# Performance work log

Hardware: AMD Instinct MI355X
Metric: run time of the kernel (lower is better)

Reference implementation:

```python
import jax, jax.numpy as jnp
import numpy as np

B, C, T, F = 8, 256, 256, 128
D, H, HEADS, K = 64, 128, 4, 8
I = D * K  # unfold channel dim = D*8


def _conv2d(x, w, b, stride=1, pad=0):
    y = jax.lax.conv_general_dilated(x, w, (stride, stride), [(pad, pad), (pad, pad)],
                                     dimension_numbers=('NCHW', 'OIHW', 'NCHW'))
    return y + b[None, :, None, None]


def _convT(x, w, b, strides):
    y = jax.lax.conv_transpose(x, w, strides, 'VALID', dimension_numbers=('NCHW', 'OIHW', 'NCHW'))
    return y + b[None, :, None, None]


def _sru_dir(x, Wx, bf, br, Whw):
    # x: (N, L, I). SRU: all matmuls precomputed, only elementwise recurrence in scan.
    u = jnp.einsum('nli,ih->nlh', x, Wx)  # (N, L, 3H)
    xt, fp, rp = jnp.split(u, 3, axis=-1)
    f = jax.nn.sigmoid(fp + bf)
    r = jax.nn.sigmoid(rp + br)
    xhw = jnp.einsum('nli,ih->nlh', x, Whw)  # highway projection (I != H)

    def step(c, inp):
        xt_t, f_t, r_t, xhw_t = inp
        c = f_t * c + (1.0 - f_t) * xt_t
        h = r_t * c + (1.0 - r_t) * xhw_t
        return c, h

    c0 = jnp.zeros((x.shape[0], bf.shape[-1]), x.dtype)
    seq = tuple(jnp.swapaxes(a, 0, 1) for a in (xt, f, r, xhw))  # (L, N, H)
    _, hs = jax.lax.scan(step, c0, seq)
    return jnp.swapaxes(hs, 0, 1)  # (N, L, H)


def _sru_bidir(x, Wx, bf, br, Whw):
    hf = _sru_dir(x, Wx[0], bf[0], br[0], Whw[0])
    hb = _sru_dir(x[:, ::-1], Wx[1], bf[1], br[1], Whw[1])[:, ::-1]
    return jnp.concatenate([hf, hb], axis=-1)  # (N, L, 2H)


def _unfold_last(x, k):
    # nn.Unfold(kernel=(1,k)) over last axis: (B,D,T,F) -> (B, D*k, T, F-k+1)
    L = x.shape[-1] - k + 1
    p = jnp.stack([x[..., i:i + L] for i in range(k)], axis=2)  # (B, D, k, T, L)
    b, d = x.shape[0], x.shape[1]
    return p.reshape(b, d * k, x.shape[2], L)


def _pathway(ag, Wx, bf, br, Whw, pw, pb, ctw, ctb):
    # unfold -> bidirectional SRU over last axis -> proj -> ConvTranspose2d(I->D, kernel (1,8))
    b, d, t, f = ag.shape
    L = f - K + 1
    u = _unfold_last(ag, K)                                  # (B, I, t, L)
    seq = u.transpose(0, 2, 3, 1).reshape(b * t, L, d * K)   # scan along unfolded axis
    h = _sru_bidir(seq, Wx, bf, br, Whw)                     # (b*t, L, 2H)
    z = h @ pw + pb                                          # (b*t, L, I)
    z = z.reshape(b, t, L, d * K).transpose(0, 3, 1, 2)      # (B, I, t, L)
    return _convT(z, ctw, ctb, (1, 1))                       # (B, D, t, f)


def _attention(x, qkv_w, qkv_b, ow, ob):
    b, d, t, f = x.shape
    n = t * f
    tok = x.reshape(b, d, n).transpose(0, 2, 1)  # (B, N, D)
    qkv = tok @ qkv_w + qkv_b
    q, k, v = jnp.split(qkv, 3, axis=-1)
    dh = d // HEADS
    sp = lambda a: a.reshape(b, n, HEADS, dh).transpose(0, 2, 1, 3)
    q, k, v = sp(q), sp(k), sp(v)
    s = jnp.einsum('bhnd,bhmd->bhnm', q, k) / jnp.sqrt(jnp.asarray(dh, x.dtype))
    a = jax.nn.softmax(s, axis=-1)
    o = jnp.einsum('bhnm,bhmd->bhnd', a, v).transpose(0, 2, 1, 3).reshape(b, n, d)
    o = o @ ow + ob
    return o.transpose(0, 2, 1).reshape(b, d, t, f)


def _forward(A, compress_w, compress_b, down_w0, down_b0, down_w1, down_b1,
             f_Wx, f_bf, f_br, f_Whw, f_proj_w, f_proj_b, f_ct_w, f_ct_b,
             t_Wx, t_bf, t_br, t_Whw, t_proj_w, t_proj_b, t_ct_w, t_ct_b,
             qkv_w, qkv_b, out_w, out_b, up_w0, up_b0, up_w1, up_b1, final_w, final_b):
    # Compressor: 1x1 conv C->D then 2 strided downsample units
    x0 = _conv2d(A, compress_w, compress_b)                              # (B,D,T,F)
    x1 = jax.nn.relu(_conv2d(x0, down_w0, down_b0, stride=2, pad=1))     # (B,D,T/2,F/2)
    x2 = jax.nn.relu(_conv2d(x1, down_w1, down_b1, stride=2, pad=1))     # (B,D,T/4,F/4)
    ag = x2
    # Dual path: frequency scan then time scan, with residuals as in _dual_path
    freq_out = _pathway(ag, f_Wx, f_bf, f_br, f_Whw, f_proj_w, f_proj_b, f_ct_w, f_ct_b) + ag
    agt = ag.transpose(0, 1, 3, 2)  # scan over time axis
    time_out = _pathway(agt, t_Wx, t_bf, t_br, t_Whw, t_proj_w, t_proj_b, t_ct_w, t_ct_b).transpose(0, 1, 3, 2) + freq_out
    # TF self-attention with residual
    dp = _attention(time_out, qkv_w, qkv_b, out_w, out_b) + time_out
    # U-Net style reconstruction with skips, project back to C
    y = _convT(dp, up_w0, up_b0, (2, 2)) + x1
    y = _convT(y, up_w1, up_b1, (2, 2)) + x0
    return _conv2d(y, final_w, final_b)                                  # (B,C,T,F)


def setup_inputs() -> dict:
    key = jax.random.key(0)
    ks = iter(jax.random.split(key, 64))

    def p(shape, scale=0.05):
        return jax.random.normal(next(ks), shape, dtype=jnp.float32) * scale

    inp = dict(
        A=jax.random.normal(next(ks), (B, C, T, F), dtype=jnp.float32),
        compress_w=p((D, C, 1, 1)), compress_b=p((D,)),
        down_w0=p((D, D, 3, 3)), down_b0=p((D,)),
        down_w1=p((D, D, 3, 3)), down_b1=p((D,)),
        f_Wx=p((2, I, 3 * H)), f_bf=p((2, H)), f_br=p((2, H)), f_Whw=p((2, I, H)),
        f_proj_w=p((2 * H, I)), f_proj_b=p((I,)), f_ct_w=p((D, I, 1, K)), f_ct_b=p((D,)),
        t_Wx=p((2, I, 3 * H)), t_bf=p((2, H)), t_br=p((2, H)), t_Whw=p((2, I, H)),
        t_proj_w=p((2 * H, I)), t_proj_b=p((I,)), t_ct_w=p((D, I, 1, K)), t_ct_b=p((D,)),
        qkv_w=p((D, 3 * D)), qkv_b=p((3 * D,)), out_w=p((D, D)), out_b=p((D,)),
        up_w0=p((D, D, 2, 2)), up_b0=p((D,)),
        up_w1=p((D, D, 2, 2)), up_b1=p((D,)),
        final_w=p((C, D, 1, 1)), final_b=p((C,)),
    )
    return inp


def reference(A, compress_w, compress_b, down_w0, down_b0, down_w1, down_b1,
              f_Wx, f_bf, f_br, f_Whw, f_proj_w, f_proj_b, f_ct_w, f_ct_b,
              t_Wx, t_bf, t_br, t_Whw, t_proj_w, t_proj_b, t_ct_w, t_ct_b,
              qkv_w, qkv_b, out_w, out_b, up_w0, up_b0, up_w1, up_b1, final_w, final_b):
    return _forward(A, compress_w, compress_b, down_w0, down_b0, down_w1, down_b1,
                    f_Wx, f_bf, f_br, f_Whw, f_proj_w, f_proj_b, f_ct_w, f_ct_b,
                    t_Wx, t_bf, t_br, t_Whw, t_proj_w, t_proj_b, t_ct_w, t_ct_b,
                    qkv_w, qkv_b, out_w, out_b, up_w0, up_b0, up_w1, up_b1, final_w, final_b)
```

## Files before the change

kernel.cpp:

```cpp
#include <hip/hip_runtime.h>

#define BB 8
#define CC 256
#define TT 256
#define FF 128
#define DD 64
#define HH 128
#define NHEADS 4
#define KK 8
#define II 512
#define T2 128
#define F2 64
#define T4 64
#define F4 32
#define P4 2048

#define LF 25
#define LT 57
#define MF (512*LF)
#define MT (256*LT)

typedef __attribute__((ext_vector_type(8))) short bf16x8;
typedef __attribute__((ext_vector_type(4))) float f32x4;

__device__ __forceinline__ ushort f2b(float x) {
    unsigned u = __float_as_uint(x);
    unsigned r = (u + 0x7FFFu + ((u >> 16) & 1u)) >> 16;
    return (ushort)r;
}
__device__ __forceinline__ float b2f(ushort x) {
    return __uint_as_float(((unsigned)x) << 16);
}
__device__ __forceinline__ unsigned cvtpk_bf16(float lo, float hi) {
    unsigned r;
    asm("v_cvt_pk_bf16_f32 %0, %1, %2" : "=v"(r) : "v"(lo), "v"(hi));
    return r;
}

__global__ __launch_bounds__(256) void pack_all_k(
    const float* __restrict__ cw, const float* __restrict__ fw,
    const float* __restrict__ upw0, const float* __restrict__ upw1,
    const float* __restrict__ qkv_w, const float* __restrict__ ow,
    const float* __restrict__ dw0, const float* __restrict__ dw1,
    const float* __restrict__ f_pw, const float* __restrict__ t_pw,
    const float* __restrict__ f_ctw, const float* __restrict__ t_ctw,
    const float* __restrict__ f_Wx, const float* __restrict__ f_Whw,
    const float* __restrict__ t_Wx, const float* __restrict__ t_Whw,
    ushort* __restrict__ cw16, ushort* __restrict__ fw16,
    ushort* __restrict__ WupT0, ushort* __restrict__ WupT1,
    ushort* __restrict__ qkvwT, ushort* __restrict__ owT,
    ushort* __restrict__ WT9d0, ushort* __restrict__ WT9d1,
    ushort* __restrict__ pwF16, ushort* __restrict__ pwT16,
    ushort* __restrict__ WctF, ushort* __restrict__ WctT_,
    ushort* __restrict__ WcatF, ushort* __restrict__ WcatTm)
{
    int bid = blockIdx.x, tid = threadIdx.x;
    if (bid < 64)        { int g = bid * 256 + tid; cw16[g] = f2b(cw[g]); return; }
    if (bid < 128)       { int g = (bid - 64) * 256 + tid; fw16[g] = f2b(fw[g]); return; }
    if (bid < 256) {
        const float* w = (bid < 192) ? upw0 : upw1;
        ushort* O = (bid < 192) ? WupT0 : WupT1;
        int g = ((bid - 128) & 63) * 256 + tid;
        int c = g & 63; int n = g >> 6;
        int parity = n >> 6, d = n & 63;
        O[g] = f2b(w[((d * 64 + c) * 2 + (1 - (parity >> 1))) * 2 + (1 - (parity & 1))]);
        return;
    }
    if (bid < 304) {
        int g = (bid - 256) * 256 + tid;
        int k = g & 63, n = g >> 6;
        qkvwT[g] = f2b(qkv_w[k * 192 + n]); return;
    }
    if (bid < 320) {
        int g = (bid - 304) * 256 + tid;
        int k = g & 63, n = g >> 6;
        owT[g] = f2b(ow[k * 64 + n]); return;
    }
    if (bid < 608) {
        const float* w = (bid < 464) ? dw0 : dw1;
        ushort* O = (bid < 464) ? WT9d0 : WT9d1;
        int g = ((bid - 320) % 144) * 256 + tid;
        int c = g & 63; int rest = g >> 6;
        int d = rest & 63; int tap = rest >> 6;
        O[g] = f2b(w[(d * 64 + c) * 9 + tap]); return;
    }
    if (bid < 1632) {
        const float* w = (bid < 1120) ? f_pw : t_pw;
        ushort* O = (bid < 1120) ? pwF16 : pwT16;
        int g = ((bid - 608) % 512) * 256 + tid;
        O[g] = f2b(w[g]); return;
    }
    if (bid < 3680) {
        const float* ctw = (bid < 2656) ? f_ctw : t_ctw;
        ushort* O = (bid < 2656) ? WctF : WctT_;
        int g = ((bid - 1632) % 1024) * 256 + tid;
        int k = g & 511; int n = g >> 9;
        int tap = n >> 6, d = n & 63;
        O[g] = f2b(ctw[((d * 512) + k) * 8 + tap]); return;
    }
    {
        const float* Wx  = (bid < 5728) ? f_Wx  : t_Wx;
        const float* Whw = (bid < 5728) ? f_Whw : t_Whw;
        ushort* O = (bid < 5728) ? WcatF : WcatTm;
        int g = ((bid - 3680) % 2048) * 256 + tid;
        int k = g & 511; int n = g >> 9;
        int dir = n >> 9; int c = n & 511;
        float v = (c < 384) ? Wx[(dir * 512 + k) * 384 + c]
                            : Whw[(dir * 512 + k) * 128 + (c - 384)];
        O[g] = f2b(v);
    }
}

__global__ __launch_bounds__(256) void w3_gemm_k(
    const ushort* __restrict__ pwA, const ushort* __restrict__ wctA,
    const ushort* __restrict__ pwB, const ushort* __restrict__ wctB,
    ushort* __restrict__ w3A, ushort* __restrict__ w3B)
{
    const int M = 256, K = 512;
    const ushort* A16  = blockIdx.z ? pwB  : pwA;
    const ushort* BT16 = blockIdx.z ? wctB : wctA;
    ushort* C16        = blockIdx.z ? w3B  : w3A;
    __shared__ ushort As[128][40];
    __shared__ ushort Bs[128][40];
    int m0 = blockIdx.y * 128, n0 = blockIdx.x * 128;
    int tid = threadIdx.x;
    int wave = tid >> 6, lane = tid & 63;
    int wm = (wave & 1) * 64, wn = (wave >> 1) * 64;
    int l15 = lane & 15, lhi = lane >> 4;
    f32x4 acc[4][4] = {};
    int rs = tid >> 2, qs = tid & 3;

    for (int k0 = 0; k0 < K; k0 += 32) {
        *(uint4*)&As[rs][qs * 8]      = *(const uint4*)(A16 + (long long)(m0 + rs) * K + k0 + qs * 8);
        *(uint4*)&As[rs + 64][qs * 8] = *(const uint4*)(A16 + (long long)(m0 + rs + 64) * K + k0 + qs * 8);
        *(uint4*)&Bs[rs][qs * 8]      = *(const uint4*)(BT16 + (long long)(n0 + rs) * K + k0 + qs * 8);
        *(uint4*)&Bs[rs + 64][qs * 8] = *(const uint4*)(BT16 + (long long)(n0 + rs + 64) * K + k0 + qs * 8);
        __syncthreads();
        bf16x8 af[4], bfr[4];
#pragma unroll
        for (int fr = 0; fr < 4; ++fr)
            af[fr] = *(const bf16x8*)&As[wm + fr * 16 + l15][lhi * 8];
#pragma unroll
        for (int fc = 0; fc < 4; ++fc)
            bfr[fc] = *(const bf16x8*)&Bs[wn + fc * 16 + l15][lhi * 8];
#pragma unroll
        for (int fr = 0; fr < 4; ++fr)
#pragma unroll
            for (int fc = 0; fc < 4; ++fc)
                acc[fr][fc] = __builtin_amdgcn_mfma_f32_16x16x32_bf16(af[fr], bfr[fc], acc[fr][fc], 0, 0, 0);
        __syncthreads();
    }
#pragma unroll
    for (int fr = 0; fr < 4; ++fr)
#pragma unroll
        for (int fc = 0; fc < 4; ++fc) {
            int col = n0 + wn + fc * 16 + l15;
#pragma unroll
            for (int r = 0; r < 4; ++r) {
                int row = m0 + wm + fr * 16 + lhi * 4 + r;
                C16[(long long)col * M + row] = f2b(acc[fr][fc][r]);
            }
        }
}

__global__ void bias3_red_k(const float* __restrict__ pbF, const float* __restrict__ ctwF,
                            const float* __restrict__ pbT, const float* __restrict__ ctwT,
                            float* __restrict__ b3F, float* __restrict__ b3T)
{
    int n = blockIdx.x; int path = blockIdx.y;
    const float* pb  = path ? pbT  : pbF;
    const float* ctw = path ? ctwT : ctwF;
    float* b3        = path ? b3T  : b3F;
    int d = n & 63, tap = n >> 6;
    int tid = threadIdx.x;
    float s = 0.f;
    for (int i = tid; i < 512; i += 256)
        s += pb[i] * ctw[(d * 512 + i) * 8 + tap];
    __shared__ float red[256];
    red[tid] = s; __syncthreads();
    for (int st = 128; st > 0; st >>= 1) {
        if (tid < st) red[tid] += red[tid + st];
        __syncthreads();
    }
    if (tid == 0) b3[n] = red[0];
}

__global__ void unfold_both_k(const float* __restrict__ ag,
                              ushort* __restrict__ uF, ushort* __restrict__ uT)
{
    long long gid = (long long)blockIdx.x * blockDim.x + threadIdx.x;
    if (gid < (long long)MF * II) {
        int ch = (int)(gid & 511); int row = (int)(gid >> 9);
        int b = row / (T4 * LF); int rem = row - b * (T4 * LF);
        int t = rem / LF; int l = rem - t * LF;
        int d = ch >> 3, i = ch & 7;
        uF[gid] = f2b(ag[((long long)((b * DD + d) * T4 + t)) * F4 + l + i]);
    } else {
        long long g2 = gid - (long long)MF * II;
        int ch = (int)(g2 & 511); int row = (int)(g2 >> 9);
        int b = row / (F4 * LT); int rem = row - b * (F4 * LT);
        int tt = rem / LT; int l = rem - tt * LT;
        int d = ch >> 3, i = ch & 7;
        uT[g2] = f2b(ag[((long long)((b * DD + d) * T4 + (l + i))) * F4 + tt]);
    }
}

__global__ __launch_bounds__(256) void gates_fused_k(
    const ushort* __restrict__ uF, const ushort* __restrict__ uT,
    const ushort* __restrict__ WF, const ushort* __restrict__ WTm,
    float* __restrict__ GxtF, float* __restrict__ GxhF,
    ushort* __restrict__ GfF, ushort* __restrict__ GrF,
    float* __restrict__ GxtT, float* __restrict__ GxhT,
    ushort* __restrict__ GfT, ushort* __restrict__ GrT,
    const float* __restrict__ f_bf, const float* __restrict__ f_br,
    const float* __restrict__ t_bf, const float* __restrict__ t_br)
{
    __shared__ ushort As[128][40];
    __shared__ ushort Bs[128][40];
    const int K = 512;
    int by = blockIdx.y;
    bool tp = by >= 100;
    const ushort* A16 = tp ? uT : uF;
    const ushort* WT  = tp ? WTm : WF;
    float* Gxt = tp ? GxtT : GxtF;
    float* Gxh = tp ? GxhT : GxhF;
    ushort* Gf = tp ? GfT : GfF;
    ushort* Gr = tp ? GrT : GrF;
    const float* bfw = tp ? t_bf : f_bf;
    const float* brw = tp ? t_br : f_br;
    int m0 = (tp ? by - 100 : by) * 128;
    int n0 = blockIdx.x * 128;
    int tid = threadIdx.x, wave = tid >> 6, lane = tid & 63;
    int wm = (wave & 1) * 64, wn = (wave >> 1) * 64;
    int l15 = lane & 15, lhi = lane >> 4;
    f32x4 acc[4][4] = {};
    int rs = tid >> 2, qs = tid & 3;

    for (int k0 = 0; k0 < K; k0 += 32) {
        *(uint4*)&As[rs][qs * 8]      = *(const uint4*)(A16 + (long long)(m0 + rs) * K + k0 + qs * 8);
        *(uint4*)&As[rs + 64][qs * 8] = *(const uint4*)(A16 + (long long)(m0 + rs + 64) * K + k0 + qs * 8);
        *(uint4*)&Bs[rs][qs * 8]      = *(const uint4*)(WT + (long long)(n0 + rs) * K + k0 + qs * 8);
        *(uint4*)&Bs[rs + 64][qs * 8] = *(const uint4*)(WT + (long long)(n0 + rs + 64) * K + k0 + qs * 8);
        __syncthreads();
        bf16x8 af[4], bfr[4];
#pragma unroll
        for (int fr = 0; fr < 4; ++fr)
            af[fr] = *(const bf16x8*)&As[wm + fr * 16 + l15][lhi * 8];
#pragma unroll
        for (int fc = 0; fc < 4; ++fc)
            bfr[fc] = *(const bf16x8*)&Bs[wn + fc * 16 + l15][lhi * 8];
#pragma unroll
        for (int fr = 0; fr < 4; ++fr)
#pragma unroll
            for (int fc = 0; fc < 4; ++fc)
                acc[fr][fc] = __builtin_amdgcn_mfma_f32_16x16x32_bf16(af[fr], bfr[fc], acc[fr][fc], 0, 0, 0);
        __syncthreads();
    }
#pragma unroll
    for (int fc = 0; fc < 4; ++fc) {
        int col = n0 + wn + fc * 16 + l15;
        int dir = col >> 9, c = col & 511;
        int cls = c >> 7, h = c & 127;
        int dh = dir * 128 + h;
#pragma unroll
        for (int fr = 0; fr < 4; ++fr) {
#pragma unroll
            for (int r = 0; r < 4; ++r) {
                int row = m0 + wm + fr * 16 + lhi * 4 + r;
                long long idx = (long long)row * 256 + dh;
                float v = acc[fr][fc][r];
                if (cls == 0)      Gxt[idx] = v;
                else if (cls == 3) Gxh[idx] = v;
                else if (cls == 1) Gf[idx] = f2b(1.f / (1.f + __expf(-(v + bfw[dh]))));
                else               Gr[idx] = f2b(1.f / (1.f + __expf(-(v + brw[dh]))));
            }
        }
    }
}

__global__ void sru_scan_both_k(
    const float* __restrict__ GxtF, const float* __restrict__ GxhF,
    const ushort* __restrict__ GfF, const ushort* __restrict__ GrF,
    ushort* __restrict__ hF,
    const float* __restrict__ GxtT, const float* __restrict__ GxhT,
    const ushort* __restrict__ GfT, const ushort* __restrict__ GrT,
    ushort* __restrict__ hT)
{
    int gid = blockIdx.x * blockDim.x + threadIdx.x;
    const float *Gxt, *Gxh; const ushort *Gf, *Gr; ushort* hout; int L;
    if (gid < 512 * 256) {
        Gxt = GxtF; Gxh = GxhF; Gf = GfF; Gr = GrF; hout = hF; L = LF;
    } else {
        gid -= 512 * 256;
        Gxt = GxtT; Gxh = GxhT; Gf = GfT; Gr = GrT; hout = hT; L = LT;
    }
    int h = gid & 127; int dir = (gid >> 7) & 1; int n = gid >> 8;
    int dh = dir * 128 + h;
    float c = 0.f;
    for (int s = 0; s < L; ++s) {
        int l = dir ? (L - 1 - s) : s;
        long long off = (long long)(n * L + l) * 256 + dh;
        float xt = Gxt[off], xh = Gxh[off];
        float f = b2f(Gf[off]);
        float r = b2f(Gr[off]);
        c = f * c + (1.f - f) * xt;
        float hv = r * c + (1.f - r) * xh;
        hout[off] = f2b(hv);
    }
}

__global__ __launch_bounds__(256) void gemmW_both_k(
    const ushort* __restrict__ hF, const ushort* __restrict__ W3F,
    float* __restrict__ YF, const float* __restrict__ b3F,
    const ushort* __restrict__ hT, const ushort* __restrict__ W3T,
    float* __restrict__ YT, const float* __restrict__ b3T)
{
    __shared__ ushort As[128][40];
    __shared__ ushort Bs[128][40];
    const int N = 512, K = 256;
    int by = blockIdx.y;
    bool tp = by >= 100;
    const ushort* A16 = tp ? hT : hF;
    const ushort* WT  = tp ? W3T : W3F;
    float* C          = tp ? YT : YF;
    const float* bias = tp ? b3T : b3F;
    int m0 = (tp ? by - 100 : by) * 128;
    int n0 = blockIdx.x * 128;
    int tid = threadIdx.x, wave = tid >> 6, lane = tid & 63;
    int wm = (wave & 1) * 64, wn = (wave >> 1) * 64;
    int l15 = lane & 15, lhi = lane >> 4;
    f32x4 acc[4][4] = {};
    int rs = tid >> 2, qs = tid & 3;

    for (int k0 = 0; k0 < K; k0 += 32) {
        *(uint4*)&As[rs][qs * 8]      = *(const uint4*)(A16 + (long long)(m0 + rs) * K + k0 + qs * 8);
        *(uint4*)&As[rs + 64][qs * 8] = *(const uint4*)(A16 + (long long)(m0 + rs + 64) * K + k0 + qs * 8);
        *(uint4*)&Bs[rs][qs * 8]      = *(const uint4*)(WT + (long long)(n0 + rs) * K + k0 + qs * 8);
        *(uint4*)&Bs[rs + 64][qs * 8] = *(const uint4*)(WT + (long long)(n0 + rs + 64) * K + k0 + qs * 8);
        __syncthreads();
        bf16x8 af[4], bfr[4];
#pragma unroll
        for (int fr = 0; fr < 4; ++fr)
            af[fr] = *(const bf16x8*)&As[wm + fr * 16 + l15][lhi * 8];
#pragma unroll
        for (int fc = 0; fc < 4; ++fc)
            bfr[fc] = *(const bf16x8*)&Bs[wn + fc * 16 + l15][lhi * 8];
#pragma unroll
        for (int fr = 0; fr < 4; ++fr)
#pragma unroll
            for (int fc = 0; fc < 4; ++fc)
                acc[fr][fc] = __builtin_amdgcn_mfma_f32_16x16x32_bf16(af[fr], bfr[fc], acc[fr][fc], 0, 0, 0);
        __syncthreads();
    }
#pragma unroll
    for (int fc = 0; fc < 4; ++fc) {
        int col = n0 + wn + fc * 16 + l15;
        float bv = bias[col];
#pragma unroll
        for (int fr = 0; fr < 4; ++fr) {
#pragma unroll
            for (int r = 0; r < 4; ++r) {
                int row = m0 + wm + fr * 16 + lhi * 4 + r;
                C[(long long)row * N + col] = acc[fr][fc][r] + bv;
            }
        }
    }
}

template<int BN>
__global__ __launch_bounds__(256) void mfma_nchw_k(
    const float* __restrict__ X, const ushort* __restrict__ WT,
    const float* __restrict__ bias, float* __restrict__ Y,
    int P, int N, int K)
{
    constexpr int FC = BN / 32;
    __shared__ ushort As[128][40];
    int p0 = blockIdx.x * 128;
    int n0 = blockIdx.y * BN;
    int b  = blockIdx.z;
    int tid = threadIdx.x, wave = tid >> 6, lane = tid & 63;
    int l15 = lane & 15, lhi = lane >> 4;
    int wm = (wave & 1) * 64, wn = (wave >> 1) * (BN / 2);
    f32x4 acc[4][FC] = {};
    const float* Xb = X + (long long)b * K * P;
    int kk_s = tid >> 3, pq_s = tid & 7;

    for (int k0 = 0; k0 < K; k0 += 32) {
        const float* xr = Xb + (long long)(k0 + kk_s) * P + p0;
#pragma unroll
        for (int j = 0; j < 4; ++j) {
            float4 v = *(const float4*)(xr + j * 32 + pq_s * 4);
            int pp = j * 32 + pq_s * 4;
            As[pp][kk_s]     = f2b(v.x);
            As[pp + 1][kk_s] = f2b(v.y);
            As[pp + 2][kk_s] = f2b(v.z);
            As[pp + 3][kk_s] = f2b(v.w);
        }
        __syncthreads();
        bf16x8 af[4], bfr[FC];
#pragma unroll
        for (int fr = 0; fr < 4; ++fr)
            af[fr] = *(const bf16x8*)&As[wm + fr * 16 + l15][lhi * 8];
#pragma unroll
        for (int fc = 0; fc < FC; ++fc)
            bfr[fc] = *(const bf16x8*)(WT + (long long)(n0 + wn + fc * 16 + l15) * K + k0 + lhi * 8);
#pragma unroll
        for (int fr = 0; fr < 4; ++fr)
#pragma unroll
            for (int fc = 0; fc < FC; ++fc)
                acc[fr][fc] = __builtin_amdgcn_mfma_f32_16x16x32_bf16(af[fr], bfr[fc], acc[fr][fc], 0, 0, 0);
        __syncthreads();
    }
#pragma unroll
    for (int fc = 0; fc < FC; ++fc) {
        int n = n0 + wn + fc * 16 + l15;
        float bv = bias[n];
        float* yr = Y + ((long long)(b * N + n)) * P + p0 + wm + lhi * 4;
#pragma unroll
        for (int fr = 0; fr < 4; ++fr) {
            float4 o;
            o.x = acc[fr][fc][0] + bv;
            o.y = acc[fr][fc][1] + bv;
            o.z = acc[fr][fc][2] + bv;
            o.w = acc[fr][fc][3] + bv;
            *(float4*)(yr + fr * 16) = o;
        }
    }
}

__global__ __launch_bounds__(256) void mfma_nchw16_k(
    const ushort* __restrict__ X, const ushort* __restrict__ WT,
    const float* __restrict__ bias, float* __restrict__ Y,
    int P, int N, int K)
{
    constexpr int BN = 128, FC = 4;
    __shared__ ushort As[128][40];
    int p0 = blockIdx.x * 128;
    int n0 = blockIdx.y * BN;
    int b  = blockIdx.z;
    int tid = threadIdx.x, wave = tid >> 6, lane = tid & 63;
    int l15 = lane & 15, lhi = lane >> 4;
    int wm = (wave & 1) * 64, wn = (wave >> 1) * (BN / 2);
    f32x4 acc[4][FC] = {};
    const ushort* Xb = X + (long long)b * K * P;
    int kk_s = tid >> 3, pq_s = tid & 7;

    for (int k0 = 0; k0 < K; k0 += 32) {
        const ushort* xr = Xb + (long long)(k0 + kk_s) * P + p0 + pq_s * 16;
#pragma unroll
        for (int j = 0; j < 2; ++j) {
            uint4 v = *(const uint4*)(xr + j * 8);
            const ushort* e = (const ushort*)&v;
            int pp = pq_s * 16 + j * 8;
#pragma unroll
            for (int t = 0; t < 8; ++t) As[pp + t][kk_s] = e[t];
        }
        __syncthreads();
        bf16x8 af[4], bfr[FC];
#pragma unroll
        for (int fr = 0; fr < 4; ++fr)
            af[fr] = *(const bf16x8*)&As[wm + fr * 16 + l15][lhi * 8];
#pragma unroll
        for (int fc = 0; fc < FC; ++fc)
            bfr[fc] = *(const bf16x8*)(WT + (long long)(n0 + wn + fc * 16 + l15) * K + k0 + lhi * 8);
#pragma unroll
        for (int fr = 0; fr < 4; ++fr)
#pragma unroll
            for (int fc = 0; fc < FC; ++fc)
                acc[fr][fc] = __builtin_amdgcn_mfma_f32_16x16x32_bf16(af[fr], bfr[fc], acc[fr][fc], 0, 0, 0);
        __syncthreads();
    }
#pragma unroll
    for (int fc = 0; fc < FC; ++fc) {
        int n = n0 + wn + fc * 16 + l15;
        float bv = bias[n];
        float* yr = Y + ((long long)(b * N + n)) * P + p0 + wm + lhi * 4;
#pragma unroll
        for (int fr = 0; fr < 4; ++fr) {
            float4 o;
            o.x = acc[fr][fc][0] + bv;
            o.y = acc[fr][fc][1] + bv;
            o.z = acc[fr][fc][2] + bv;
            o.w = acc[fr][fc][3] + bv;
            *(float4*)(yr + fr * 16) = o;
        }
    }
}

__global__ __launch_bounds__(256) void down_mfma_k(
    const float* __restrict__ in, const ushort* __restrict__ WT9,
    const float* __restrict__ bias, float* __restrict__ out,
    int Hi, int Wi)
{
    __shared__ ushort Is[289][64];
    int Ho = Hi >> 1, Wo = Wi >> 1;
    int ntx = Wo >> 3, nty = Ho >> 3;
    int tx = blockIdx.x % ntx; int rest = blockIdx.x / ntx;
    int ty = rest % nty; int b = rest / nty;
    int oy0 = ty * 8, ox0 = tx * 8;
    int iy0 = oy0 * 2 - 1, ix0 = ox0 * 2 - 1;
    int tid = threadIdx.x, wave = tid >> 6, lane = tid & 63;
    int l15 = lane & 15, lhi = lane >> 4;
    int wm = (wave & 1) * 32, wn = (wave >> 1) * 32;

    const float* ib = in + (long long)b * 64 * Hi * Wi;
    for (int i = tid; i < 289 * 64; i += 256) {
        int c = i / 289; int sp = i - c * 289;
        int r = sp / 17; int s = sp - r * 17;
        int iy = iy0 + r, ix = ix0 + s;
        float v = 0.f;
        if (iy >= 0 && iy < Hi && ix >= 0 && ix < Wi)
            v = ib[(long long)c * Hi * Wi + (long long)iy * Wi + ix];
        Is[sp][c ^ ((sp & 7) << 3)] = f2b(v);
    }
    __syncthreads();

    f32x4 acc[2][2] = {};
#pragma unroll
    for (int tap = 0; tap < 9; ++tap) {
        int kh = tap / 3, kw = tap - kh * 3;
#pragma unroll
        for (int half = 0; half < 2; ++half) {
            int c0 = half * 32 + lhi * 8;
            bf16x8 af[2], bw[2];
#pragma unroll
            for (int fr = 0; fr < 2; ++fr) {
                int p = wm + fr * 16 + l15;
                int sp = (2 * (p >> 3) + kh) * 17 + 2 * (p & 7) + kw;
                af[fr] = *(const bf16x8*)&Is[sp][c0 ^ ((sp & 7) << 3)];
            }
#pragma unroll
            for (int fc = 0; fc < 2; ++fc) {
                int d = wn + fc * 16 + l15;
                bw[fc] = *(const bf16x8*)(WT9 + (tap * 64 + d) * 64 + c0);
            }
#pragma unroll
            for (int fr = 0; fr < 2; ++fr)
#pragma unroll
                for (int fc = 0; fc < 2; ++fc)
                    acc[fr][fc] = __builtin_amdgcn_mfma_f32_16x16x32_bf16(af[fr], bw[fc], acc[fr][fc], 0, 0, 0);
        }
    }
#pragma unroll
    for (int fc = 0; fc < 2; ++fc) {
        int d = wn + fc * 16 + l15;
        float bv = bias[d];
        long long obase = ((long long)(b * 64 + d)) * Ho * Wo;
#pragma unroll
        for (int fr = 0; fr < 2; ++fr) {
#pragma unroll
            for (int r = 0; r < 4; ++r) {
                int p = wm + fr * 16 + lhi * 4 + r;
                int py = p >> 3, px = p & 7;
                out[obase + (long long)(oy0 + py) * Wo + ox0 + px] =
                    fmaxf(acc[fr][fc][r] + bv, 0.f);
            }
        }
    }
}

template<int OUT16>
__global__ __launch_bounds__(256) void up_mfma_k(
    const float* __restrict__ in, const ushort* __restrict__ WT,
    const float* __restrict__ bias, const float* __restrict__ resid,
    float* __restrict__ out, ushort* __restrict__ o16, int P, int wsh)
{
    __shared__ ushort As[128][72];
    int p0 = blockIdx.x * 128;
    int n0 = blockIdx.y * 128;
    int b  = blockIdx.z;
    int tid = threadIdx.x, wave = tid >> 6, lane = tid & 63;
    int l15 = lane & 15, lhi = lane >> 4;
    int wm = (wave & 1) * 64, wn = (wave >> 1) * 64;
    int Wi = 1 << wsh;
    int Ho = ((P >> wsh) << 1), Wo = Wi << 1;

    int kk_s = tid >> 3, pq_s = tid & 7;
#pragma unroll
    for (int h = 0; h < 2; ++h) {
        int k = h * 32 + kk_s;
        const float* xr = in + ((long long)(b * 64 + k)) * P + p0 + pq_s * 16;
#pragma unroll
        for (int j = 0; j < 4; ++j) {
            float4 v = *(const float4*)(xr + j * 4);
            int pp = pq_s * 16 + j * 4;
            As[pp][k]     = f2b(v.x);
            As[pp + 1][k] = f2b(v.y);
            As[pp + 2][k] = f2b(v.z);
            As[pp + 3][k] = f2b(v.w);
        }
    }
    __syncthreads();

    f32x4 acc[4][4] = {};
#pragma unroll
    for (int c = 0; c < 2; ++c) {
        bf16x8 af[4], bfr[4];
#pragma unroll
        for (int fr = 0; fr < 4; ++fr)
            af[fr] = *(const bf16x8*)&As[wm + fr * 16 + l15][c * 32 + lhi * 8];
#pragma unroll
        for (int fc = 0; fc < 4; ++fc)
            bfr[fc] = *(const bf16x8*)(WT + (long long)(n0 + wn + fc * 16 + l15) * 64 + c * 32 + lhi * 8);
#pragma unroll
        for (int fr = 0; fr < 4; ++fr)
#pragma unroll
            for (int fc = 0; fc < 4; ++fc)
                acc[fr][fc] = __builtin_amdgcn_mfma_f32_16x16x32_bf16(af[fr], bfr[fc], acc[fr][fc], 0, 0, 0);
    }

#pragma unroll
    for (int fc = 0; fc < 4; ++fc) {
        int n = n0 + wn + fc * 16 + l15;
        int parity = n >> 6, d = n & 63;
        int py = parity >> 1, px = parity & 1;
        float bv = bias[d];
        const long long obase = ((long long)(b * 64 + d)) * Ho * Wo;
#pragma unroll
        for (int fr = 0; fr < 4; ++fr) {
#pragma unroll
            for (int r = 0; r < 4; ++r) {
                int p = p0 + wm + fr * 16 + lhi * 4 + r;
                int iy = p >> wsh, ix = p & (Wi - 1);
                long long oi = obase + (long long)(2 * iy + py) * Wo + 2 * ix + px;
                float v = acc[fr][fc][r] + bv + resid[oi];
                if (OUT16) o16[oi] = f2b(v);
                else       out[oi] = v;
            }
        }
    }
}

__global__ __launch_bounds__(256) void mfma_qkv_k(
    const float* __restrict__ X, const ushort* __restrict__ WT,
    const float* __restrict__ bias, ushort* __restrict__ C16)
{
    __shared__ ushort As[128][72];
    int p0 = blockIdx.x * 128;
    int b  = blockIdx.z;
    int tid = threadIdx.x, wave = tid >> 6, lane = tid & 63;
    int l15 = lane & 15, lhi = lane >> 4;
    int wm = (wave & 1) * 64, wn = (wave >> 1) * 96;

    int kk_s = tid >> 3, pq_s = tid & 7;
#pragma unroll
    for (int h = 0; h < 2; ++h) {
        int k = h * 32 + kk_s;
        const float* xr = X + ((long long)(b * 64 + k)) * P4 + p0 + pq_s * 16;
#pragma unroll
        for (int j = 0; j < 4; ++j) {
            float4 v = *(const float4*)(xr + j * 4);
            int pp = pq_s * 16 + j * 4;
            As[pp][k]     = f2b(v.x);
            As[pp + 1][k] = f2b(v.y);
            As[pp + 2][k] = f2b(v.z);
            As[pp + 3][k] = f2b(v.w);
        }
    }
    __syncthreads();

    f32x4 acc[4][6] = {};
#pragma unroll
    for (int c = 0; c < 2; ++c) {
        bf16x8 af[4], bfr[6];
#pragma unroll
        for (int fr = 0; fr < 4; ++fr)
            af[fr] = *(const bf16x8*)&As[wm + fr * 16 + l15][c * 32 + lhi * 8];
#pragma unroll
        for (int fc = 0; fc < 6; ++fc)
            bfr[fc] = *(const bf16x8*)(WT + (long long)(wn + fc * 16 + l15) * 64 + c * 32 + lhi * 8);
#pragma unroll
        for (int fr = 0; fr < 4; ++fr)
#pragma unroll
            for (int fc = 0; fc < 6; ++fc)
                acc[fr][fc] = __builtin_amdgcn_mfma_f32_16x16x32_bf16(af[fr], bfr[fc], acc[fr][fc], 0, 0, 0);
    }
#pragma unroll
    for (int fc = 0; fc < 6; ++fc) {
        int n = wn + fc * 16 + l15;
        float bv = bias[n];
#pragma unroll
        for (int fr = 0; fr < 4; ++fr)
#pragma unroll
            for (int r = 0; r < 4; ++r) {
                int p = p0 + wm + fr * 16 + lhi * 4 + r;
                C16[((long long)(b * P4 + p)) * 192 + n] = f2b(acc[fr][fc][r] + bv);
            }
    }
}

__global__ __launch_bounds__(256) void mfma_attnout_k(
    const float* __restrict__ A, const ushort* __restrict__ owT,
    const float* __restrict__ ob, const float* __restrict__ resid,
    float* __restrict__ dp)
{
    __shared__ ushort As[128][72];
    int p0 = blockIdx.x * 128;
    int b  = blockIdx.z;
    int tid = threadIdx.x, wave = tid >> 6, lane = tid & 63;
    int l15 = lane & 15, lhi = lane >> 4;
    int wm = (wave & 1) * 64, wn = (wave >> 1) * 32;

    int rs = tid >> 2, qs = tid & 3;
#pragma unroll
    for (int h = 0; h < 2; ++h) {
        int row = h * 64 + rs;
        const float* ar = A + ((long long)(b * P4 + p0 + row)) * 64 + qs * 16;
#pragma unroll
        for (int j = 0; j < 4; ++j) {
            float4 v = *(const float4*)(ar + j * 4);
            int c = qs * 16 + j * 4;
            *(unsigned*)&As[row][c]     = cvtpk_bf16(v.x, v.y);
            *(unsigned*)&As[row][c + 2] = cvtpk_bf16(v.z, v.w);
        }
    }
    __syncthreads();

    f32x4 acc[4][2] = {};
#pragma unroll
    for (int c = 0; c < 2; ++c) {
        bf16x8 af[4], bfr[2];
#pragma unroll
        for (int fr = 0; fr < 4; ++fr)
            af[fr] = *(const bf16x8*)&As[wm + fr * 16 + l15][c * 32 + lhi * 8];
#pragma unroll
        for (int fc = 0; fc < 2; ++fc)
            bfr[fc] = *(const bf16x8*)(owT + (long long)(wn + fc * 16 + l15) * 64 + c * 32 + lhi * 8);
#pragma unroll
        for (int fr = 0; fr < 4; ++fr)
#pragma unroll
            for (int fc = 0; fc < 2; ++fc)
                acc[fr][fc] = __builtin_amdgcn_mfma_f32_16x16x32_bf16(af[fr], bfr[fc], acc[fr][fc], 0, 0, 0);
    }
#pragma unroll
    for (int fc = 0; fc < 2; ++fc) {
        int n = wn + fc * 16 + l15;
        float bv = ob[n];
        long long base = ((long long)(b * 64 + n)) * P4;
#pragma unroll
        for (int fr = 0; fr < 4; ++fr) {
            int p = p0 + wm + fr * 16 + lhi * 4;
            float4 rv = *(const float4*)(resid + base + p);
            float4 o;
            o.x = acc[fr][fc][0] + bv + rv.x;
            o.y = acc[fr][fc][1] + bv + rv.y;
            o.z = acc[fr][fc][2] + bv + rv.z;
            o.w = acc[fr][fc][3] + bv + rv.w;
            *(float4*)(dp + base + p) = o;
        }
    }
}

__global__ __launch_bounds__(256) void attn_mfma_k(const ushort* __restrict__ qkv,
                                                   float* __restrict__ out)
{
    __shared__ ushort Qs[128][40];
    __shared__ ushort Ks[64][40];
    __shared__ ushort VsT[16][72];
    __shared__ ushort Ps[128][72];
    int qt = blockIdx.x, h = blockIdx.y, b = blockIdx.z;
    int tid = threadIdx.x, wave = tid >> 6, lane = tid & 63;
    int l15 = lane & 15, lhi = lane >> 4;
    int q0 = wave * 32;

    for (int i = tid; i < 1024; i += 256) {
        int row = i >> 3, c = i & 7;
        *(unsigned*)&Qs[row][16 + c * 2] = 0u;
    }
    for (int i = tid; i < 512; i += 256) {
        int row = i >> 3, c = i & 7;
        *(unsigned*)&Ks[row][16 + c * 2] = 0u;
    }
    {
        const ushort* qp = qkv + ((long long)(b * P4 + qt * 128)) * 192 + h * 16;
        for (int i = tid; i < 2048; i += 256) {
            int row = i >> 4, d = i & 15;
            Qs[row][d] = f2b(b2f(qp[row * 192 + d]) * 0.25f);
        }
    }
    __syncthreads();

    float mmax[2] = {-1e30f, -1e30f};
    float lsum[2] = {0.f, 0.f};
    f32x4 oacc[2] = {};

    for (int k0 = 0; k0 < P4; k0 += 64) {
        const ushort* kp = qkv + ((long long)(b * P4 + k0)) * 192 + 64 + h * 16;
        for (int i = tid; i < 1024; i += 256) {
            int key = i >> 4, d = i & 15;
            Ks[key][d]  = kp[key * 192 + d];
            VsT[d][key] = kp[key * 192 + 64 + d];
        }
        __syncthreads();

        bf16x8 bq[2];
        bq[0] = *(const bf16x8*)&Qs[q0 + l15][lhi * 8];
        bq[1] = *(const bf16x8*)&Qs[q0 + 16 + l15][lhi * 8];
        f32x4 s[4][2];
#pragma unroll
        for (int fr = 0; fr < 4; ++fr) {
            bf16x8 ak = *(const bf16x8*)&Ks[fr * 16 + l15][lhi * 8];
            f32x4 z = {};
            s[fr][0] = __builtin_amdgcn_mfma_f32_16x16x32_bf16(ak, bq[0], z, 0, 0, 0);
            s[fr][1] = __builtin_amdgcn_mfma_f32_16x16x32_bf16(ak, bq[1], z, 0, 0, 0);
        }
#pragma unroll
        for (int fc = 0; fc < 2; ++fc) {
            float m = s[0][fc][0];
#pragma unroll
            for (int fr = 0; fr < 4; ++fr)
#pragma unroll
                for (int r = 0; r < 4; ++r) m = fmaxf(m, s[fr][fc][r]);
            m = fmaxf(m, __shfl_xor(m, 16));
            m = fmaxf(m, __shfl_xor(m, 32));
            float nm = fmaxf(mmax[fc], m);
            float corr = __expf(mmax[fc] - nm);
            mmax[fc] = nm;
            float ps = 0.f;
#pragma unroll
            for (int fr = 0; fr < 4; ++fr)
#pragma unroll
                for (int r = 0; r < 4; ++r) {
                    float p = __expf(s[fr][fc][r] - nm);
                    s[fr][fc][r] = p;
                    ps += p;
                }
            lsum[fc] = lsum[fc] * corr + ps;
#pragma unroll
            for (int r = 0; r < 4; ++r) oacc[fc][r] *= corr;
        }
#pragma unroll
        for (int fc = 0; fc < 2; ++fc)
#pragma unroll
            for (int fr = 0; fr < 4; ++fr) {
                uint2 pk;
                pk.x = cvtpk_bf16(s[fr][fc][0], s[fr][fc][1]);
                pk.y = cvtpk_bf16(s[fr][fc][2], s[fr][fc][3]);
                *(uint2*)&Ps[q0 + fc * 16 + l15][fr * 16 + lhi * 4] = pk;
            }
#pragma unroll
        for (int ks = 0; ks < 2; ++ks) {
            bf16x8 av = *(const bf16x8*)&VsT[l15][ks * 32 + lhi * 8];
#pragma unroll
            for (int fc = 0; fc < 2; ++fc) {
                bf16x8 bp = *(const bf16x8*)&Ps[q0 + fc * 16 + l15][ks * 32 + lhi * 8];
                oacc[fc] = __builtin_amdgcn_mfma_f32_16x16x32_bf16(av, bp, oacc[fc], 0, 0, 0);
            }
        }
        __syncthreads();
    }
#pragma unroll
    for (int fc = 0; fc < 2; ++fc) {
        float L = lsum[fc];
        L += __shfl_xor(L, 16);
        L += __shfl_xor(L, 32);
        float inv = 1.f / L;
        int q = qt * 128 + q0 + fc * 16 + l15;
        float* op = out + ((long long)(b * P4 + q)) * 64 + h * 16 + lhi * 4;
#pragma unroll
        for (int r = 0; r < 4; ++r) op[r] = oacc[fc][r] * inv;
    }
}

__global__ void convt_reduce_k(const float* __restrict__ Y, const float* __restrict__ bias,
                               const float* __restrict__ resid, float* __restrict__ out,
                               int NS, int L, int FO, int swap)
{
    int gid = blockIdx.x * blockDim.x + threadIdx.x;
    int total = BB * 64 * NS * FO;
    if (gid >= total) return;
    int d = gid & 63; int rest = gid >> 6;
    int p = rest % FO; rest /= FO;
    int s = rest % NS; int b = rest / NS;
    float v = bias[d];
    long long ybase = ((long long)(b * NS + s)) * L;
#pragma unroll
    for (int tap = 0; tap < 8; ++tap) {
        int l = p + tap - 7;
        if (l >= 0 && l < L) v += Y[(ybase + l) * 512 + tap * 64 + d];
    }
    long long oi = swap ? (((long long)(b * 64 + d) * FO + p) * NS + s)
                        : (((long long)(b * 64 + d) * NS + s) * FO + p);
    out[oi] = v + resid[oi];
}

extern "C" void kernel_launch(void* const* d_in, const int* in_sizes, int n_in,
                              void* d_out, int out_size, void* d_ws, size_t ws_size,
                              hipStream_t stream)
{
    const float* A_in  = (const float*)d_in[0];
    const float* cw    = (const float*)d_in[1];
    const float* cb    = (const float*)d_in[2];
    const float* dw0   = (const float*)d_in[3];
    const float* db0   = (const float*)d_in[4];
    const float* dw1   = (const float*)d_in[5];
    const float* db1   = (const float*)d_in[6];
    const float* f_Wx  = (const float*)d_in[7];
    const float* f_bf  = (const float*)d_in[8];
    const float* f_br  = (const float*)d_in[9];
    const float* f_Whw = (const float*)d_in[10];
    const float* f_pw  = (const float*)d_in[11];
    const float* f_pb  = (const float*)d_in[12];
    const float* f_ctw = (const float*)d_in[13];
    const float* f_ctb = (const float*)d_in[14];
    const float* t_Wx  = (const float*)d_in[15];
    const float* t_bf  = (const float*)d_in[16];
    const float* t_br  = (const float*)d_in[17];
    const float* t_Whw = (const float*)d_in[18];
    const float* t_pw  = (const float*)d_in[19];
    const float* t_pb  = (const float*)d_in[20];
    const float* t_ctw = (const float*)d_in[21];
    const float* t_ctb = (const float*)d_in[22];
    const float* qkv_w = (const float*)d_in[23];
    const float* qkv_b = (const float*)d_in[24];
    const float* ow    = (const float*)d_in[25];
    const float* ob    = (const float*)d_in[26];
    const float* upw0  = (const float*)d_in[27];
    const float* upb0  = (const float*)d_in[28];
    const float* upw1  = (const float*)d_in[29];
    const float* upb1  = (const float*)d_in[30];
    const float* fw    = (const float*)d_in[31];
    const float* fb    = (const float*)d_in[32];

    float* ws  = (float*)d_ws;
    float* out = (float*)d_out;

    float* ag    = ws + 0;
    float* x1    = ws + 1048576;
    float* uFf   = ws + 5242880;
    float* uTf   = ws + 8519680;
    float* GxtF  = ws + 12255232;
    float* GxhF  = ws + 15532032;
    float* GxtT  = ws + 18808832;
    float* GxhT  = ws + 22544384;
    float* GfFf  = ws + 26279936;
    float* GrFf  = ws + 27918336;
    float* GfTf  = ws + 29556736;
    float* GrTf  = ws + 31424512;
    float* hFf   = ws + 33292288;
    float* hTf   = ws + 34930688;
    float* YF    = ws + 5242880;
    float* YT    = ws + 11796480;
    float* y016f = ws + 19267584;
    float* y1    = ws + 5242880;
    float* pwFf  = ws + 36798464;
    float* pwTf  = ws + 36864000;
    float* w3Ff  = ws + 36929536;
    float* w3Tf  = ws + 36995072;
    float* b3Ff  = ws + 37060608;
    float* b3Tf  = ws + 37061120;
    float* wctFf = ws + 37061632;
    float* wctTf = ws + 37192704;
    float* wcaFf = ws + 37323776;
    float* wcaTf = ws + 37585920;
    float* cw16f = ws + 37848064;
    float* fw16f = ws + 37856256;
    float* wup0f = ws + 37864448;
    float* wup1f = ws + 37872640;
    float* qkvwf = ws + 37880832;
    float* owtf  = ws + 37886976;
    float* wdw0f = ws + 37889024;
    float* wdw1f = ws + 37907456;
    float* fout  = ws + 37925888;
    float* tout  = ws + 38974464;
    float* qkvbf = ws + 40023040;
    float* attnO = ws + 41595904;
    float* dp    = ws + 42644480;

    ushort* uF     = (ushort*)uFf;
    ushort* uT     = (ushort*)uTf;
    ushort* GfF    = (ushort*)GfFf;
    ushort* GrF    = (ushort*)GrFf;
    ushort* GfT    = (ushort*)GfTf;
    ushort* GrT    = (ushort*)GrTf;
    ushort* hF     = (ushort*)hFf;
    ushort* hT     = (ushort*)hTf;
    ushort* y016   = (ushort*)y016f;
    ushort* pwF16  = (ushort*)pwFf;
    ushort* pwT16  = (ushort*)pwTf;
    ushort* W3F    = (ushort*)w3Ff;
    ushort* W3T_   = (ushort*)w3Tf;
    ushort* WctF   = (ushort*)wctFf;
    ushort* WctT_  = (ushort*)wctTf;
    ushort* WcatF  = (ushort*)wcaFf;
    ushort* WcatTm = (ushort*)wcaTf;
    ushort* qkv16  = (ushort*)qkvbf;
    ushort* cw16   = (ushort*)cw16f;
    ushort* fw16   = (ushort*)fw16f;
    ushort* WupT0  = (ushort*)wup0f;
    ushort* WupT1  = (ushort*)wup1f;
    ushort* qkvwT  = (ushort*)qkvwf;
    ushort* owT    = (ushort*)owtf;
    ushort* WT9d0  = (ushort*)wdw0f;
    ushort* WT9d1  = (ushort*)wdw1f;
    float*  x0     = out;

    dim3 blk(256);

    pack_all_k<<<dim3(7776), blk, 0, stream>>>(
        cw, fw, upw0, upw1, qkv_w, ow, dw0, dw1, f_pw, t_pw, f_ctw, t_ctw,
        f_Wx, f_Whw, t_Wx, t_Whw,
        cw16, fw16, WupT0, WupT1, qkvwT, owT, WT9d0, WT9d1,
        pwF16, pwT16, WctF, WctT_, WcatF, WcatTm);
    w3_gemm_k<<<dim3(4, 2, 2), blk, 0, stream>>>(pwF16, WctF, pwT16, WctT_, W3F, W3T_);
    bias3_red_k<<<dim3(512, 2), blk, 0, stream>>>(f_pb, f_ctw, t_pb, t_ctw, b3Ff, b3Tf);

    mfma_nchw_k<64><<<dim3(256, 1, 8), blk, 0, stream>>>(A_in, cw16, cb, x0, 32768, 64, 256);

    down_mfma_k<<<dim3(1024), blk, 0, stream>>>(x0, WT9d0, db0, x1, TT, FF);
    down_mfma_k<<<dim3(256), blk, 0, stream>>>(x1, WT9d1, db1, ag, T2, F2);

    unfold_both_k<<<dim3(54784), blk, 0, stream>>>(ag, uF, uT);
    gates_fused_k<<<dim3(8, 214), blk, 0, stream>>>(uF, uT, WcatF, WcatTm,
        GxtF, GxhF, GfF, GrF, GxtT, GxhT, GfT, GrT, f_bf, f_br, t_bf, t_br);
    sru_scan_both_k<<<dim3(768), blk, 0, stream>>>(GxtF, GxhF, GfF, GrF, hF,
                                                   GxtT, GxhT, GfT, GrT, hT);
    gemmW_both_k<<<dim3(4, 214), blk, 0, stream>>>(hF, W3F, YF, b3Ff,
                                                   hT, W3T_, YT, b3Tf);
    convt_reduce_k<<<dim3(4096), blk, 0, stream>>>(YF, f_ctb, ag, fout, 64, LF, 32, 0);
    convt_reduce_k<<<dim3(4096), blk, 0, stream>>>(YT, t_ctb, fout, tout, 32, LT, 64, 1);

    mfma_qkv_k<<<dim3(16, 1, 8), blk, 0, stream>>>(tout, qkvwT, qkv_b, qkv16);
    attn_mfma_k<<<dim3(16, NHEADS, BB), blk, 0, stream>>>(qkv16, attnO);
    mfma_attnout_k<<<dim3(16, 1, 8), blk, 0, stream>>>(attnO, owT, ob, tout, dp);

    up_mfma_k<0><<<dim3(16, 2, 8), blk, 0, stream>>>(dp, WupT0, upb0, x1, y1, nullptr, 2048, 5);
    up_mfma_k<1><<<dim3(64, 2, 8), blk, 0, stream>>>(y1, WupT1, upb1, x0, nullptr, y016, 8192, 6);

    mfma_nchw16_k<<<dim3(256, 2, 8), blk, 0, stream>>>(y016, fw16, fb, out, 32768, 256, 64);
}
```

Baseline: 672.1 us.

## Store SRU gate and projection intermediates in bf16 and fuse both ConvT reductions

Changes the Gxt/Gxh gate outputs and the post-SRU projection outputs Y from fp32 to bf16, which halves their memory traffic in the gates, scan, gemm and reduce kernels. It also replaces the two sequential convt_reduce launches with one dual_reduce kernel that sums the frequency and time pathway contributions, both biases and the residual in a single pass. That removes the intermediate fout buffer and one launch. The cost is lower precision on values that were previously kept in fp32.

```diff
diff --git a/kernel.cpp b/kernel.cpp
--- a/kernel.cpp
+++ b/kernel.cpp
@@ -208,9 +208,9 @@
 __global__ __launch_bounds__(256) void gates_fused_k(
     const ushort* __restrict__ uF, const ushort* __restrict__ uT,
     const ushort* __restrict__ WF, const ushort* __restrict__ WTm,
-    float* __restrict__ GxtF, float* __restrict__ GxhF,
+    ushort* __restrict__ GxtF, ushort* __restrict__ GxhF,
     ushort* __restrict__ GfF, ushort* __restrict__ GrF,
-    float* __restrict__ GxtT, float* __restrict__ GxhT,
+    ushort* __restrict__ GxtT, ushort* __restrict__ GxhT,
     ushort* __restrict__ GfT, ushort* __restrict__ GrT,
     const float* __restrict__ f_bf, const float* __restrict__ f_br,
     const float* __restrict__ t_bf, const float* __restrict__ t_br)
@@ -222,8 +222,8 @@
     bool tp = by >= 100;
     const ushort* A16 = tp ? uT : uF;
     const ushort* WT  = tp ? WTm : WF;
-    float* Gxt = tp ? GxtT : GxtF;
-    float* Gxh = tp ? GxhT : GxhF;
+    ushort* Gxt = tp ? GxtT : GxtF;
+    ushort* Gxh = tp ? GxhT : GxhF;
     ushort* Gf = tp ? GfT : GfF;
     ushort* Gr = tp ? GrT : GrF;
     const float* bfw = tp ? t_bf : f_bf;
@@ -269,8 +269,8 @@
                 int row = m0 + wm + fr * 16 + lhi * 4 + r;
                 long long idx = (long long)row * 256 + dh;
                 float v = acc[fr][fc][r];
-                if (cls == 0)      Gxt[idx] = v;
-                else if (cls == 3) Gxh[idx] = v;
+                if (cls == 0)      Gxt[idx] = f2b(v);
+                else if (cls == 3) Gxh[idx] = f2b(v);
                 else if (cls == 1) Gf[idx] = f2b(1.f / (1.f + __expf(-(v + bfw[dh]))));
                 else               Gr[idx] = f2b(1.f / (1.f + __expf(-(v + brw[dh]))));
             }
@@ -279,15 +279,15 @@
 }
 
 __global__ void sru_scan_both_k(
-    const float* __restrict__ GxtF, const float* __restrict__ GxhF,
+    const ushort* __restrict__ GxtF, const ushort* __restrict__ GxhF,
     const ushort* __restrict__ GfF, const ushort* __restrict__ GrF,
     ushort* __restrict__ hF,
-    const float* __restrict__ GxtT, const float* __restrict__ GxhT,
+    const ushort* __restrict__ GxtT, const ushort* __restrict__ GxhT,
     const ushort* __restrict__ GfT, const ushort* __restrict__ GrT,
     ushort* __restrict__ hT)
 {
     int gid = blockIdx.x * blockDim.x + threadIdx.x;
-    const float *Gxt, *Gxh; const ushort *Gf, *Gr; ushort* hout; int L;
+    const ushort *Gxt, *Gxh, *Gf, *Gr; ushort* hout; int L;
     if (gid < 512 * 256) {
         Gxt = GxtF; Gxh = GxhF; Gf = GfF; Gr = GrF; hout = hF; L = LF;
     } else {
@@ -300,7 +300,7 @@
     for (int s = 0; s < L; ++s) {
         int l = dir ? (L - 1 - s) : s;
         long long off = (long long)(n * L + l) * 256 + dh;
-        float xt = Gxt[off], xh = Gxh[off];
+        float xt = b2f(Gxt[off]), xh = b2f(Gxh[off]);
         float f = b2f(Gf[off]);
         float r = b2f(Gr[off]);
         c = f * c + (1.f - f) * xt;
@@ -311,9 +311,9 @@
 
 __global__ __launch_bounds__(256) void gemmW_both_k(
     const ushort* __restrict__ hF, const ushort* __restrict__ W3F,
-    float* __restrict__ YF, const float* __restrict__ b3F,
+    ushort* __restrict__ YF, const float* __restrict__ b3F,
     const ushort* __restrict__ hT, const ushort* __restrict__ W3T,
-    float* __restrict__ YT, const float* __restrict__ b3T)
+    ushort* __restrict__ YT, const float* __restrict__ b3T)
 {
     __shared__ ushort As[128][40];
     __shared__ ushort Bs[128][40];
@@ -322,7 +322,7 @@
     bool tp = by >= 100;
     const ushort* A16 = tp ? hT : hF;
     const ushort* WT  = tp ? W3T : W3F;
-    float* C          = tp ? YT : YF;
+    ushort* C16       = tp ? YT : YF;
     const float* bias = tp ? b3T : b3F;
     int m0 = (tp ? by - 100 : by) * 128;
     int n0 = blockIdx.x * 128;
@@ -361,10 +361,32 @@
 #pragma unroll
             for (int r = 0; r < 4; ++r) {
                 int row = m0 + wm + fr * 16 + lhi * 4 + r;
-                C[(long long)row * N + col] = acc[fr][fc][r] + bv;
+                C16[(long long)row * N + col] = f2b(acc[fr][fc][r] + bv);
             }
         }
     }
+}
+
+__global__ void dual_reduce_k(const ushort* __restrict__ YF, const ushort* __restrict__ YT,
+                              const float* __restrict__ f_ctb, const float* __restrict__ t_ctb,
+                              const float* __restrict__ ag, float* __restrict__ tout)
+{
+    int gid = blockIdx.x * blockDim.x + threadIdx.x;
+    int d = gid & 63; int rest = gid >> 6;
+    int f = rest & 31; rest >>= 5;
+    int t = rest & 63; int b = rest >> 6;
+    float v = f_ctb[d] + t_ctb[d];
+    long long ybF = ((long long)(b * 64 + t)) * LF;
+    long long ybT = ((long long)(b * 32 + f)) * LT;
+#pragma unroll
+    for (int tap = 0; tap < 8; ++tap) {
+        int lf = f + tap - 7;
+        if (lf >= 0 && lf < LF) v += b2f(YF[(ybF + lf) * 512 + tap * 64 + d]);
+        int lt = t + tap - 7;
+        if (lt >= 0 && lt < LT) v += b2f(YT[(ybT + lt) * 512 + tap * 64 + d]);
+    }
+    long long oi = (((long long)(b * 64 + d)) * 64 + t) * 32 + f;
+    tout[oi] = v + ag[oi];
 }
 
 template<int BN>
@@ -860,28 +882,6 @@
 #pragma unroll
         for (int r = 0; r < 4; ++r) op[r] = oacc[fc][r] * inv;
     }
-}
-
-__global__ void convt_reduce_k(const float* __restrict__ Y, const float* __restrict__ bias,
-                               const float* __restrict__ resid, float* __restrict__ out,
-                               int NS, int L, int FO, int swap)
-{
-    int gid = blockIdx.x * blockDim.x + threadIdx.x;
-    int total = BB * 64 * NS * FO;
-    if (gid >= total) return;
-    int d = gid & 63; int rest = gid >> 6;
-    int p = rest % FO; rest /= FO;
-    int s = rest % NS; int b = rest / NS;
-    float v = bias[d];
-    long long ybase = ((long long)(b * NS + s)) * L;
-#pragma unroll
-    for (int tap = 0; tap < 8; ++tap) {
-        int l = p + tap - 7;
-        if (l >= 0 && l < L) v += Y[(ybase + l) * 512 + tap * 64 + d];
-    }
-    long long oi = swap ? (((long long)(b * 64 + d) * FO + p) * NS + s)
-                        : (((long long)(b * 64 + d) * NS + s) * FO + p);
-    out[oi] = v + resid[oi];
 }
 
 extern "C" void kernel_launch(void* const* d_in, const int* in_sizes, int n_in,
@@ -939,10 +939,10 @@
     float* GrTf  = ws + 31424512;
     float* hFf   = ws + 33292288;
     float* hTf   = ws + 34930688;
-    float* YF    = ws + 5242880;
-    float* YT    = ws + 11796480;
+    float* YF16f = ws + 5242880;
+    float* YT16f = ws + 8519680;
     float* y016f = ws + 19267584;
-    float* y1    = ws + 5242880;
+    float* y1    = ws + 12255232;
     float* pwFf  = ws + 36798464;
     float* pwTf  = ws + 36864000;
     float* w3Ff  = ws + 36929536;
@@ -961,20 +961,25 @@
     float* owtf  = ws + 37886976;
     float* wdw0f = ws + 37889024;
     float* wdw1f = ws + 37907456;
-    float* fout  = ws + 37925888;
-    float* tout  = ws + 38974464;
-    float* qkvbf = ws + 40023040;
-    float* attnO = ws + 41595904;
-    float* dp    = ws + 42644480;
+    float* tout  = ws + 37925888;
+    float* qkvbf = ws + 38974464;
+    float* attnO = ws + 40547328;
+    float* dp    = ws + 41595904;
 
     ushort* uF     = (ushort*)uFf;
     ushort* uT     = (ushort*)uTf;
+    ushort* GxtF16 = (ushort*)GxtF;
+    ushort* GxhF16 = (ushort*)GxhF;
+    ushort* GxtT16 = (ushort*)GxtT;
+    ushort* GxhT16 = (ushort*)GxhT;
     ushort* GfF    = (ushort*)GfFf;
     ushort* GrF    = (ushort*)GrFf;
     ushort* GfT    = (ushort*)GfTf;
     ushort* GrT    = (ushort*)GrTf;
     ushort* hF     = (ushort*)hFf;
     ushort* hT     = (ushort*)hTf;
+    ushort* YF16   = (ushort*)YF16f;
+    ushort* YT16   = (ushort*)YT16f;
     ushort* y016   = (ushort*)y016f;
     ushort* pwF16  = (ushort*)pwFf;
     ushort* pwT16  = (ushort*)pwTf;
@@ -1012,13 +1017,12 @@
 
     unfold_both_k<<<dim3(54784), blk, 0, stream>>>(ag, uF, uT);
     gates_fused_k<<<dim3(8, 214), blk, 0, stream>>>(uF, uT, WcatF, WcatTm,
-        GxtF, GxhF, GfF, GrF, GxtT, GxhT, GfT, GrT, f_bf, f_br, t_bf, t_br);
-    sru_scan_both_k<<<dim3(768), blk, 0, stream>>>(GxtF, GxhF, GfF, GrF, hF,
-                                                   GxtT, GxhT, GfT, GrT, hT);
-    gemmW_both_k<<<dim3(4, 214), blk, 0, stream>>>(hF, W3F, YF, b3Ff,
-                                                   hT, W3T_, YT, b3Tf);
-    convt_reduce_k<<<dim3(4096), blk, 0, stream>>>(YF, f_ctb, ag, fout, 64, LF, 32, 0);
-    convt_reduce_k<<<dim3(4096), blk, 0, stream>>>(YT, t_ctb, fout, tout, 32, LT, 64, 1);
+        GxtF16, GxhF16, GfF, GrF, GxtT16, GxhT16, GfT, GrT, f_bf, f_br, t_bf, t_br);
+    sru_scan_both_k<<<dim3(768), blk, 0, stream>>>(GxtF16, GxhF16, GfF, GrF, hF,
+                                                   GxtT16, GxhT16, GfT, GrT, hT);
+    gemmW_both_k<<<dim3(4, 214), blk, 0, stream>>>(hF, W3F, YF16, b3Ff,
+                                                   hT, W3T_, YT16, b3Tf);
+    dual_reduce_k<<<dim3(8192), blk, 0, stream>>>(YF16, YT16, f_ctb, t_ctb, ag, tout);
 
     mfma_qkv_k<<<dim3(16, 1, 8), blk, 0, stream>>>(tout, qkvwT, qkv_b, qkv16);
     attn_mfma_k<<<dim3(16, NHEADS, BB), blk, 0, stream>>>(qkv16, attnO);
```

After: 680.2 us. No clear change (+1.2%).
